# Kernel optimization log

Hardware: AMD Instinct MI355X
Metric: run time of the kernel (lower is better)

The kernel has to match this reference:

```python
import jax, jax.numpy as jnp
import numpy as np

E = 16          # num_local_experts
K = 4           # experts_per_token
H = 2048        # hidden_size
I = 2048        # intermediate_size
LIMIT = 7.0     # swiglu_limit
ALPHA = 1.702   # glu_alpha


def setup_inputs() -> dict:
    key = jax.random.key(0)
    ks = jax.random.split(key, 9)
    int8 = lambda k, shp: jax.random.randint(k, shp, -127, 128).astype(jnp.float32)
    return {
        "hidden_states": jax.random.normal(ks[0], (1024, H), dtype=jnp.float32),
        "router_logits": jax.random.normal(ks[1], (1024, E), dtype=jnp.float32),
        "gate_up_proj": int8(ks[2], (E, H, 2 * I)),                      # int8 values in f32
        "gate_up_proj_scale": jax.random.uniform(ks[3], (E, 2 * I), minval=0.5, maxval=1.5) * 0.002,
        "gate_up_proj_bias": jax.random.normal(ks[4], (E, 2 * I), dtype=jnp.float32) * 0.01,
        "gate_up_smooth_scale": jnp.ones((E, I), dtype=jnp.float32),
        "down_proj": int8(ks[5], (E, I, H)),
        "down_proj_scale": jax.random.uniform(ks[6], (E, H), minval=0.5, maxval=1.5) * 0.002,
        "down_proj_bias": jax.random.normal(ks[7], (E, H), dtype=jnp.float32) * 0.01,
    }


def _dyn_quant(x):
    # per-token symmetric int8 dynamic quant (npu_dynamic_quant)
    scale = jnp.maximum(jnp.max(jnp.abs(x), axis=-1, keepdims=True) / 127.0, 1e-8)
    q = jnp.clip(jnp.round(x / scale), -127.0, 127.0)
    return q, scale


def reference(hidden_states, router_logits, gate_up_proj, gate_up_proj_scale,
              gate_up_proj_bias, gate_up_smooth_scale, down_proj,
              down_proj_scale, down_proj_bias):
    T = hidden_states.shape[0]
    C = (2 * T * K) // E

    # --- gating (npu_moe_gating_top_k: softmax + top-k, then renormalize) ---
    probs = jax.nn.softmax(router_logits, axis=-1)
    topk_w, topk_i = jax.lax.top_k(probs, K)                 # [T,K]
    topk_w = topk_w / jnp.sum(topk_w, axis=-1, keepdims=True)

    # --- per-token dynamic quant ---
    x_q, x_scale = _dyn_quant(hidden_states)                 # [T,H], [T,1]

    # --- dispatch (npu_moe_init_routing_v2): token-major expansion, capacity buckets ---
    flat_e = topk_i.reshape(-1)                              # [T*K] expert id per row
    flat_w = topk_w.reshape(-1)                              # [T*K]
    src = jnp.arange(T * K) // K                             # [T*K] source token
    onehot = jax.nn.one_hot(flat_e, E, dtype=jnp.int32)      # [T*K,E]
    pos = jnp.sum(jnp.cumsum(onehot, axis=0) * onehot, axis=1) - 1  # position within expert
    valid = pos < C
    slot = flat_e * C + jnp.where(valid, pos, 0)             # unique for valid rows
    vf = valid.astype(x_q.dtype)[:, None]
    x_disp = jnp.zeros((E * C, H), x_q.dtype).at[slot].add(x_q[src] * vf)
    s_disp = jnp.zeros((E * C, 1), x_scale.dtype).at[slot].add(x_scale[src] * vf)
    x_disp = x_disp.reshape(E, C, H)
    s_disp = s_disp.reshape(E, C, 1)

    gu_i32 = jnp.einsum('ech,ehf->ecf', x_disp, gate_up_proj)          # [E,C,2I]
    y = gu_i32 * s_disp * gate_up_proj_scale[:, None, :] + gate_up_proj_bias[:, None, :]

    # --- gpt-oss swiglu (activate_left, clamp_limit, alpha=1.702, glu_bias=1.0) ---
    gate = jnp.minimum(y[..., :I], LIMIT)
    up = jnp.clip(y[..., I:], -LIMIT, LIMIT)
    act = gate * jax.nn.sigmoid(ALPHA * gate) * (up + 1.0)
    act = act * gate_up_smooth_scale[:, None, :]

    # --- requant + grouped GEMM 2 + dequant ---
    h_q, h_scale = _dyn_quant(act)                                     # [E,C,I], [E,C,1]
    z_i32 = jnp.einsum('eci,eih->ech', h_q, down_proj)                 # [E,C,H]
    z = z_i32 * h_scale * down_proj_scale[:, None, :] + down_proj_bias[:, None, :]

    # --- combine (npu_moe_finalize_routing): weighted scatter-add per source token ---
    gathered = z.reshape(E * C, H)[slot]                               # [T*K,H]
    out = jnp.zeros((T, H), z.dtype).at[src].add(flat_w[:, None] * vf * gathered)
    return out
```

## Files before the change

### kernel.cpp

```cpp
#include <hip/hip_runtime.h>
#include <stdint.h>
#include <stddef.h>

#define T_TOK 1024
#define NE    16
#define TOPK  4
#define HID   2048
#define INTER 2048
#define CAP   512
#define GLIMIT 7.0f
#define GALPHA 1.702f

#define BM  128
#define BK  32
#define LDP 40

typedef __attribute__((ext_vector_type(8))) _Float16 half8;
typedef __attribute__((ext_vector_type(4))) float     f32x4;

__global__ __launch_bounds__(256) void gating_kernel(
    const float* __restrict__ logits, int* __restrict__ topki, float* __restrict__ topkw)
{
    int t = blockIdx.x * 256 + threadIdx.x;
    if (t >= T_TOK) return;
    float l[NE];
#pragma unroll
    for (int e = 0; e < NE; e++) l[e] = logits[t * NE + e];
    unsigned used = 0;
    float val[TOPK]; int idx[TOPK];
#pragma unroll
    for (int k = 0; k < TOPK; k++) {
        float bv = -3.4e38f; int bi = 0;
#pragma unroll
        for (int e = 0; e < NE; e++) {
            bool ok = (((used >> e) & 1u) == 0u) && (l[e] > bv);
            bv = ok ? l[e] : bv;
            bi = ok ? e : bi;
        }
        used |= (1u << bi); idx[k] = bi; val[k] = bv;
    }
    float m = val[0];
    float s = 0.f, w[TOPK];
#pragma unroll
    for (int k = 0; k < TOPK; k++) { w[k] = expf(val[k] - m); s += w[k]; }
    float inv = 1.0f / s;
#pragma unroll
    for (int k = 0; k < TOPK; k++) { topki[t * TOPK + k] = idx[k]; topkw[t * TOPK + k] = w[k] * inv; }
}

__global__ __launch_bounds__(256) void quant_x_kernel(
    const float* __restrict__ x, _Float16* __restrict__ xq, float* __restrict__ xs)
{
    int t = blockIdx.x;
    const float* row = x + (size_t)t * HID;
    __shared__ float red[256];
    float amax = 0.f;
    for (int i = threadIdx.x; i < HID; i += 256) amax = fmaxf(amax, fabsf(row[i]));
    red[threadIdx.x] = amax; __syncthreads();
    for (int s = 128; s > 0; s >>= 1) {
        if (threadIdx.x < s) red[threadIdx.x] = fmaxf(red[threadIdx.x], red[threadIdx.x + s]);
        __syncthreads();
    }
    float scale = fmaxf(red[0] / 127.0f, 1e-8f);
    if (threadIdx.x == 0) xs[t] = scale;
    for (int i = threadIdx.x; i < HID; i += 256) {
        float q = rintf(row[i] / scale);
        q = fminf(fmaxf(q, -127.f), 127.f);
        xq[(size_t)t * HID + i] = (_Float16)q;
    }
}

__global__ __launch_bounds__(1024) void routing_kernel(
    const int* __restrict__ topki, const float* __restrict__ topkw,
    int* __restrict__ row_src, float* __restrict__ row_w, int* __restrict__ counts)
{
    int wv = threadIdx.x >> 6;
    int lane = threadIdx.x & 63;
    int base = 0;
    for (int r0 = 0; r0 < T_TOK * TOPK; r0 += 64) {
        int r = r0 + lane;
        int e = topki[r];
        unsigned long long mask = __ballot(e == wv);
        int pre = __popcll(mask & ((1ULL << lane) - 1ULL));
        if (e == wv) {
            int pos = base + pre;
            if (pos < CAP) {
                row_src[wv * CAP + pos] = r >> 2;
                row_w[wv * CAP + pos] = topkw[r];
            }
        }
        base += __popcll(mask);
    }
    if (lane == 0) counts[wv] = (base < CAP) ? base : CAP;
}

__global__ __launch_bounds__(256) void gemm1_kernel(
    const _Float16* __restrict__ xq, const float* __restrict__ xs,
    const int* __restrict__ row_src, const int* __restrict__ counts,
    const float* __restrict__ gup, const float* __restrict__ gus,
    const float* __restrict__ gub, const float* __restrict__ smo,
    float* __restrict__ act)
{
    int nt = blockIdx.x;
    int mt = blockIdx.y;
    int e  = blockIdx.z;
    int count = counts[e];
    int m0 = mt * BM;
    if (m0 >= count) return;

    __shared__ _Float16 sA[BM * LDP];
    __shared__ _Float16 sB[128 * LDP];

    int t = threadIdx.x;
    int lane = t & 63, w = t >> 6;
    int n16 = lane & 15, quad = lane >> 4;

    int aM = t >> 1, aHalf = t & 1;
    int agr = m0 + aM;
    const _Float16* aptr = nullptr;
    if (agr < count) aptr = xq + (size_t)row_src[e * CAP + agr] * HID;

    f32x4 acc[2][8];
#pragma unroll
    for (int i = 0; i < 2; i++)
#pragma unroll
        for (int j = 0; j < 8; j++) acc[i][j] = (f32x4)0.0f;

    const float* gbase = gup + (size_t)e * HID * (2 * INTER);

    for (int k0 = 0; k0 < HID; k0 += BK) {
        __syncthreads();
        {
            int4 v0, v1;
            v0.x = v0.y = v0.z = v0.w = 0; v1 = v0;
            if (aptr) {
                const int4* s4 = (const int4*)(aptr + k0 + aHalf * 16);
                v0 = s4[0]; v1 = s4[1];
            }
            int4* d4 = (int4*)&sA[aM * LDP + aHalf * 16];
            d4[0] = v0; d4[1] = v1;
        }
        {
            int n = t & 63;
            int kr = (t >> 6) * 8;
#pragma unroll
            for (int h = 0; h < 2; h++) {
                const float* src = gbase + (size_t)(k0 + kr) * (2 * INTER) + h * INTER + nt * 64 + n;
#pragma unroll
                for (int i = 0; i < 8; i++)
                    sB[(h * 64 + n) * LDP + kr + i] = (_Float16)src[(size_t)i * (2 * INTER)];
            }
        }
        __syncthreads();

        half8 af[2], bfr[8];
#pragma unroll
        for (int mf = 0; mf < 2; mf++)
            af[mf] = *(const half8*)&sA[(w * 32 + mf * 16 + n16) * LDP + quad * 8];
#pragma unroll
        for (int nf = 0; nf < 8; nf++)
            bfr[nf] = *(const half8*)&sB[(nf * 16 + n16) * LDP + quad * 8];
#pragma unroll
        for (int mf = 0; mf < 2; mf++)
#pragma unroll
            for (int nf = 0; nf < 8; nf++)
                acc[mf][nf] = __builtin_amdgcn_mfma_f32_16x16x32_f16(af[mf], bfr[nf], acc[mf][nf], 0, 0, 0);
    }

    const float* gsc = gus + (size_t)e * (2 * INTER);
    const float* gbi = gub + (size_t)e * (2 * INTER);
    const float* sms = smo + (size_t)e * INTER;
#pragma unroll
    for (int mf = 0; mf < 2; mf++) {
#pragma unroll
        for (int r = 0; r < 4; r++) {
            int gr = m0 + w * 32 + mf * 16 + quad * 4 + r;
            if (gr >= count) continue;
            float srow = xs[row_src[e * CAP + gr]];
            float* arow = act + (size_t)(e * CAP + gr) * INTER;
#pragma unroll
            for (int g = 0; g < 4; g++) {
                int col = nt * 64 + g * 16 + n16;
                float yg = acc[mf][g][r]     * srow * gsc[col]         + gbi[col];
                float yu = acc[mf][g + 4][r] * srow * gsc[INTER + col] + gbi[INTER + col];
                float gate = fminf(yg, GLIMIT);
                float up   = fminf(fmaxf(yu, -GLIMIT), GLIMIT);
                float sig  = 1.0f / (1.0f + expf(-GALPHA * gate));
                arow[col] = gate * sig * (up + 1.0f) * sms[col];
            }
        }
    }
}

__global__ __launch_bounds__(256) void requant_kernel(
    const float* __restrict__ act, const int* __restrict__ counts,
    _Float16* __restrict__ hq, float* __restrict__ hs)
{
    int b = blockIdx.x;
    int e = b >> 9, c = b & (CAP - 1);
    if (c >= counts[e]) return;
    const float* row = act + (size_t)b * INTER;
    __shared__ float red[256];
    float amax = 0.f;
    for (int i = threadIdx.x; i < INTER; i += 256) amax = fmaxf(amax, fabsf(row[i]));
    red[threadIdx.x] = amax; __syncthreads();
    for (int s = 128; s > 0; s >>= 1) {
        if (threadIdx.x < s) red[threadIdx.x] = fmaxf(red[threadIdx.x], red[threadIdx.x + s]);
        __syncthreads();
    }
    float scale = fmaxf(red[0] / 127.0f, 1e-8f);
    if (threadIdx.x == 0) hs[b] = scale;
    for (int i = threadIdx.x; i < INTER; i += 256) {
        float q = rintf(row[i] / scale);
        q = fminf(fmaxf(q, -127.f), 127.f);
        hq[(size_t)b * INTER + i] = (_Float16)q;
    }
}

__global__ __launch_bounds__(256) void gemm2_kernel(
    const _Float16* __restrict__ hq, const float* __restrict__ hs,
    const int* __restrict__ row_src, const float* __restrict__ row_w,
    const int* __restrict__ counts, const float* __restrict__ dwn,
    const float* __restrict__ dsc, const float* __restrict__ dbi,
    float* __restrict__ out)
{
    int nt = blockIdx.x;
    int mt = blockIdx.y;
    int e  = blockIdx.z;
    int count = counts[e];
    int m0 = mt * BM;
    if (m0 >= count) return;

    __shared__ _Float16 sA[BM * LDP];
    __shared__ _Float16 sB[128 * LDP];

    int t = threadIdx.x;
    int lane = t & 63, w = t >> 6;
    int n16 = lane & 15, quad = lane >> 4;

    int aM = t >> 1, aHalf = t & 1;
    int agr = m0 + aM;
    const _Float16* aptr = nullptr;
    if (agr < count) aptr = hq + (size_t)(e * CAP + agr) * INTER;

    f32x4 acc[2][8];
#pragma unroll
    for (int i = 0; i < 2; i++)
#pragma unroll
        for (int j = 0; j < 8; j++) acc[i][j] = (f32x4)0.0f;

    const float* bbase = dwn + (size_t)e * INTER * HID;

    for (int k0 = 0; k0 < INTER; k0 += BK) {
        __syncthreads();
        {
            int4 v0, v1;
            v0.x = v0.y = v0.z = v0.w = 0; v1 = v0;
            if (aptr) {
                const int4* s4 = (const int4*)(aptr + k0 + aHalf * 16);
                v0 = s4[0]; v1 = s4[1];
            }
            int4* d4 = (int4*)&sA[aM * LDP + aHalf * 16];
            d4[0] = v0; d4[1] = v1;
        }
        {
            int n = t & 127;
            int kr = (t >> 7) * 16;
            const float* src = bbase + (size_t)(k0 + kr) * HID + nt * 128 + n;
#pragma unroll
            for (int i = 0; i < 16; i++)
                sB[n * LDP + kr + i] = (_Float16)src[(size_t)i * HID];
        }
        __syncthreads();

        half8 af[2], bfr[8];
#pragma unroll
        for (int mf = 0; mf < 2; mf++)
            af[mf] = *(const half8*)&sA[(w * 32 + mf * 16 + n16) * LDP + quad * 8];
#pragma unroll
        for (int nf = 0; nf < 8; nf++)
            bfr[nf] = *(const half8*)&sB[(nf * 16 + n16) * LDP + quad * 8];
#pragma unroll
        for (int mf = 0; mf < 2; mf++)
#pragma unroll
            for (int nf = 0; nf < 8; nf++)
                acc[mf][nf] = __builtin_amdgcn_mfma_f32_16x16x32_f16(af[mf], bfr[nf], acc[mf][nf], 0, 0, 0);
    }

    const float* dscE = dsc + (size_t)e * HID;
    const float* dbiE = dbi + (size_t)e * HID;
#pragma unroll
    for (int mf = 0; mf < 2; mf++) {
#pragma unroll
        for (int r = 0; r < 4; r++) {
            int gr = m0 + w * 32 + mf * 16 + quad * 4 + r;
            if (gr >= count) continue;
            int ri = e * CAP + gr;
            float hsr = hs[ri];
            float wr  = row_w[ri];
            float* orow = out + (size_t)row_src[ri] * HID;
#pragma unroll
            for (int nf = 0; nf < 8; nf++) {
                int col = nt * 128 + nf * 16 + n16;
                float z = acc[mf][nf][r] * hsr * dscE[col] + dbiE[col];
                atomicAdd(&orow[col], wr * z);
            }
        }
    }
}

extern "C" void kernel_launch(void* const* d_in, const int* in_sizes, int n_in,
                              void* d_out, int out_size, void* d_ws, size_t ws_size,
                              hipStream_t stream)
{
    (void)in_sizes; (void)n_in; (void)out_size; (void)ws_size;
    const float* x   = (const float*)d_in[0];
    const float* rl  = (const float*)d_in[1];
    const float* gup = (const float*)d_in[2];
    const float* gus = (const float*)d_in[3];
    const float* gub = (const float*)d_in[4];
    const float* smo = (const float*)d_in[5];
    const float* dwn = (const float*)d_in[6];
    const float* dsc = (const float*)d_in[7];
    const float* dbi = (const float*)d_in[8];
    float* out = (float*)d_out;

    char* p = (char*)d_ws;
    auto carve = [&](size_t bytes) -> char* {
        char* r = p; p += (bytes + 255) & ~(size_t)255; return r;
    };
    _Float16* xq   = (_Float16*)carve((size_t)T_TOK * HID * 2);
    float* xs      = (float*)carve((size_t)T_TOK * 4);
    int* topki     = (int*)carve((size_t)T_TOK * TOPK * 4);
    float* topkw   = (float*)carve((size_t)T_TOK * TOPK * 4);
    int* counts    = (int*)carve((size_t)NE * 4);
    int* rsrc      = (int*)carve((size_t)NE * CAP * 4);
    float* rw      = (float*)carve((size_t)NE * CAP * 4);
    float* actb    = (float*)carve((size_t)NE * CAP * INTER * 4);
    _Float16* hq   = (_Float16*)carve((size_t)NE * CAP * INTER * 2);
    float* hsb     = (float*)carve((size_t)NE * CAP * 4);

    hipMemsetAsync(d_out, 0, (size_t)T_TOK * HID * 4, stream);
    gating_kernel<<<dim3((T_TOK + 255) / 256), 256, 0, stream>>>(rl, topki, topkw);
    quant_x_kernel<<<dim3(T_TOK), 256, 0, stream>>>(x, xq, xs);
    routing_kernel<<<dim3(1), 1024, 0, stream>>>(topki, topkw, rsrc, rw, counts);
    gemm1_kernel<<<dim3(INTER / 64, CAP / BM, NE), 256, 0, stream>>>(
        xq, xs, rsrc, counts, gup, gus, gub, smo, actb);
    requant_kernel<<<dim3(NE * CAP), 256, 0, stream>>>(actb, counts, hq, hsb);
    gemm2_kernel<<<dim3(HID / 128, CAP / BM, NE), 256, 0, stream>>>(
        hq, hsb, rsrc, rw, counts, dwn, dsc, dbi, out);
}
```

Baseline: 1.078 ms.

## Retile MoE GEMMs to 256-row M tiles with vectorized weight loads and warp skipping

Both grouped GEMMs now use 512-thread blocks with a 256-row M tile, BK of 64 and a 64-column N tile. The f32 weight tiles are loaded as coalesced float4 rows and packed as half2 pairs into LDS, replacing the strided per-element scalar loads. Because the M tile covers the whole expected token count, the weight matrices are streamed fewer times per expert. Warps whose rows lie beyond the expert's count skip their MFMA work. Costs are more LDS per block, fewer MFMAs per wave per K-step, and possible LDS bank conflicts from the transposed half2 stores.

```diff
diff --git a/kernel.cpp b/kernel.cpp
--- a/kernel.cpp
+++ b/kernel.cpp
@@ -11,11 +11,13 @@
 #define GLIMIT 7.0f
 #define GALPHA 1.702f
 
-#define BM  128
-#define BK  32
-#define LDP 40
+#define BM  256
+#define BK  64
+#define PA  88
+#define PB  88
 
 typedef __attribute__((ext_vector_type(8))) _Float16 half8;
+typedef __attribute__((ext_vector_type(2))) _Float16 half2v;
 typedef __attribute__((ext_vector_type(4))) float     f32x4;
 
 __global__ __launch_bounds__(256) void gating_kernel(
@@ -94,7 +96,7 @@
     if (lane == 0) counts[wv] = (base < CAP) ? base : CAP;
 }
 
-__global__ __launch_bounds__(256) void gemm1_kernel(
+__global__ __launch_bounds__(512) void gemm1_kernel(
     const _Float16* __restrict__ xq, const float* __restrict__ xs,
     const int* __restrict__ row_src, const int* __restrict__ counts,
     const float* __restrict__ gup, const float* __restrict__ gus,
@@ -108,65 +110,82 @@
     int m0 = mt * BM;
     if (m0 >= count) return;
 
-    __shared__ _Float16 sA[BM * LDP];
-    __shared__ _Float16 sB[128 * LDP];
+    __shared__ _Float16 sA[BM * PA];
+    __shared__ _Float16 sB[64 * PB];
 
     int t = threadIdx.x;
     int lane = t & 63, w = t >> 6;
     int n16 = lane & 15, quad = lane >> 4;
 
-    int aM = t >> 1, aHalf = t & 1;
-    int agr = m0 + aM;
+    int arow = t >> 1, ahalf = t & 1;
     const _Float16* aptr = nullptr;
-    if (agr < count) aptr = xq + (size_t)row_src[e * CAP + agr] * HID;
-
-    f32x4 acc[2][8];
+    {
+        int agr = m0 + arow;
+        if (agr < count) aptr = xq + (size_t)row_src[e * CAP + agr] * HID;
+    }
+    _Float16* sAw = &sA[arow * PA + ahalf * 32];
+
+    int colq = t & 15;
+    int kp   = t >> 4;
+    int c64  = colq * 4;
+    const float* bptr = gup + (size_t)e * HID * (2 * INTER)
+                      + (size_t)(c64 >> 5) * INTER + nt * 32 + (c64 & 31);
+    _Float16* sBw = &sB[c64 * PB + kp * 2];
+
+    f32x4 acc[2][4];
 #pragma unroll
     for (int i = 0; i < 2; i++)
 #pragma unroll
-        for (int j = 0; j < 8; j++) acc[i][j] = (f32x4)0.0f;
-
-    const float* gbase = gup + (size_t)e * HID * (2 * INTER);
+        for (int j = 0; j < 4; j++) acc[i][j] = (f32x4)0.0f;
+
+    bool wactive = (m0 + w * 32) < count;
 
     for (int k0 = 0; k0 < HID; k0 += BK) {
         __syncthreads();
         {
-            int4 v0, v1;
-            v0.x = v0.y = v0.z = v0.w = 0; v1 = v0;
+            int4 v0 = {0,0,0,0}, v1 = v0, v2 = v0, v3 = v0;
             if (aptr) {
-                const int4* s4 = (const int4*)(aptr + k0 + aHalf * 16);
-                v0 = s4[0]; v1 = s4[1];
-            }
-            int4* d4 = (int4*)&sA[aM * LDP + aHalf * 16];
-            d4[0] = v0; d4[1] = v1;
+                const int4* s4 = (const int4*)(aptr + k0 + ahalf * 32);
+                v0 = s4[0]; v1 = s4[1]; v2 = s4[2]; v3 = s4[3];
+            }
+            int4* d = (int4*)sAw;
+            d[0] = v0; d[1] = v1; d[2] = v2; d[3] = v3;
         }
         {
-            int n = t & 63;
-            int kr = (t >> 6) * 8;
-#pragma unroll
-            for (int h = 0; h < 2; h++) {
-                const float* src = gbase + (size_t)(k0 + kr) * (2 * INTER) + h * INTER + nt * 64 + n;
-#pragma unroll
-                for (int i = 0; i < 8; i++)
-                    sB[(h * 64 + n) * LDP + kr + i] = (_Float16)src[(size_t)i * (2 * INTER)];
-            }
-        }
-        __syncthreads();
-
-        half8 af[2], bfr[8];
-#pragma unroll
-        for (int mf = 0; mf < 2; mf++)
-            af[mf] = *(const half8*)&sA[(w * 32 + mf * 16 + n16) * LDP + quad * 8];
-#pragma unroll
-        for (int nf = 0; nf < 8; nf++)
-            bfr[nf] = *(const half8*)&sB[(nf * 16 + n16) * LDP + quad * 8];
-#pragma unroll
-        for (int mf = 0; mf < 2; mf++)
-#pragma unroll
-            for (int nf = 0; nf < 8; nf++)
-                acc[mf][nf] = __builtin_amdgcn_mfma_f32_16x16x32_f16(af[mf], bfr[nf], acc[mf][nf], 0, 0, 0);
-    }
-
+            const float* s = bptr + (size_t)(k0 + kp * 2) * (2 * INTER);
+            float4 r0 = *(const float4*)(s);
+            float4 r1 = *(const float4*)(s + 2 * INTER);
+            half2v w0 = { (_Float16)r0.x, (_Float16)r1.x };
+            half2v w1 = { (_Float16)r0.y, (_Float16)r1.y };
+            half2v w2 = { (_Float16)r0.z, (_Float16)r1.z };
+            half2v w3 = { (_Float16)r0.w, (_Float16)r1.w };
+            *(half2v*)(sBw + 0 * PB) = w0;
+            *(half2v*)(sBw + 1 * PB) = w1;
+            *(half2v*)(sBw + 2 * PB) = w2;
+            *(half2v*)(sBw + 3 * PB) = w3;
+        }
+        __syncthreads();
+
+        if (wactive) {
+#pragma unroll
+            for (int ks = 0; ks < 2; ks++) {
+                half8 af[2], bfr[4];
+#pragma unroll
+                for (int mf = 0; mf < 2; mf++)
+                    af[mf] = *(const half8*)&sA[(w * 32 + mf * 16 + n16) * PA + ks * 32 + quad * 8];
+#pragma unroll
+                for (int nf = 0; nf < 4; nf++)
+                    bfr[nf] = *(const half8*)&sB[(nf * 16 + n16) * PB + ks * 32 + quad * 8];
+#pragma unroll
+                for (int mf = 0; mf < 2; mf++)
+#pragma unroll
+                    for (int nf = 0; nf < 4; nf++)
+                        acc[mf][nf] = __builtin_amdgcn_mfma_f32_16x16x32_f16(af[mf], bfr[nf], acc[mf][nf], 0, 0, 0);
+            }
+        }
+    }
+
+    if (!wactive) return;
     const float* gsc = gus + (size_t)e * (2 * INTER);
     const float* gbi = gub + (size_t)e * (2 * INTER);
     const float* sms = smo + (size_t)e * INTER;
@@ -177,16 +196,16 @@
             int gr = m0 + w * 32 + mf * 16 + quad * 4 + r;
             if (gr >= count) continue;
             float srow = xs[row_src[e * CAP + gr]];
-            float* arow = act + (size_t)(e * CAP + gr) * INTER;
-#pragma unroll
-            for (int g = 0; g < 4; g++) {
-                int col = nt * 64 + g * 16 + n16;
+            float* arow_p = act + (size_t)(e * CAP + gr) * INTER;
+#pragma unroll
+            for (int g = 0; g < 2; g++) {
+                int col = nt * 32 + g * 16 + n16;
                 float yg = acc[mf][g][r]     * srow * gsc[col]         + gbi[col];
-                float yu = acc[mf][g + 4][r] * srow * gsc[INTER + col] + gbi[INTER + col];
+                float yu = acc[mf][g + 2][r] * srow * gsc[INTER + col] + gbi[INTER + col];
                 float gate = fminf(yg, GLIMIT);
                 float up   = fminf(fmaxf(yu, -GLIMIT), GLIMIT);
                 float sig  = 1.0f / (1.0f + expf(-GALPHA * gate));
-                arow[col] = gate * sig * (up + 1.0f) * sms[col];
+                arow_p[col] = gate * sig * (up + 1.0f) * sms[col];
             }
         }
     }
@@ -217,7 +236,7 @@
     }
 }
 
-__global__ __launch_bounds__(256) void gemm2_kernel(
+__global__ __launch_bounds__(512) void gemm2_kernel(
     const _Float16* __restrict__ hq, const float* __restrict__ hs,
     const int* __restrict__ row_src, const float* __restrict__ row_w,
     const int* __restrict__ counts, const float* __restrict__ dwn,
@@ -231,62 +250,81 @@
     int m0 = mt * BM;
     if (m0 >= count) return;
 
-    __shared__ _Float16 sA[BM * LDP];
-    __shared__ _Float16 sB[128 * LDP];
+    __shared__ _Float16 sA[BM * PA];
+    __shared__ _Float16 sB[64 * PB];
 
     int t = threadIdx.x;
     int lane = t & 63, w = t >> 6;
     int n16 = lane & 15, quad = lane >> 4;
 
-    int aM = t >> 1, aHalf = t & 1;
-    int agr = m0 + aM;
+    int arow = t >> 1, ahalf = t & 1;
     const _Float16* aptr = nullptr;
-    if (agr < count) aptr = hq + (size_t)(e * CAP + agr) * INTER;
-
-    f32x4 acc[2][8];
+    {
+        int agr = m0 + arow;
+        if (agr < count) aptr = hq + (size_t)(e * CAP + agr) * INTER;
+    }
+    _Float16* sAw = &sA[arow * PA + ahalf * 32];
+
+    int colq = t & 15;
+    int kp   = t >> 4;
+    int c64  = colq * 4;
+    const float* bptr = dwn + (size_t)e * INTER * HID + nt * 64 + c64;
+    _Float16* sBw = &sB[c64 * PB + kp * 2];
+
+    f32x4 acc[2][4];
 #pragma unroll
     for (int i = 0; i < 2; i++)
 #pragma unroll
-        for (int j = 0; j < 8; j++) acc[i][j] = (f32x4)0.0f;
-
-    const float* bbase = dwn + (size_t)e * INTER * HID;
+        for (int j = 0; j < 4; j++) acc[i][j] = (f32x4)0.0f;
+
+    bool wactive = (m0 + w * 32) < count;
 
     for (int k0 = 0; k0 < INTER; k0 += BK) {
         __syncthreads();
         {
-            int4 v0, v1;
-            v0.x = v0.y = v0.z = v0.w = 0; v1 = v0;
+            int4 v0 = {0,0,0,0}, v1 = v0, v2 = v0, v3 = v0;
             if (aptr) {
-                const int4* s4 = (const int4*)(aptr + k0 + aHalf * 16);
-                v0 = s4[0]; v1 = s4[1];
-            }
-            int4* d4 = (int4*)&sA[aM * LDP + aHalf * 16];
-            d4[0] = v0; d4[1] = v1;
+                const int4* s4 = (const int4*)(aptr + k0 + ahalf * 32);
+                v0 = s4[0]; v1 = s4[1]; v2 = s4[2]; v3 = s4[3];
+            }
+            int4* d = (int4*)sAw;
+            d[0] = v0; d[1] = v1; d[2] = v2; d[3] = v3;
         }
         {
-            int n = t & 127;
-            int kr = (t >> 7) * 16;
-            const float* src = bbase + (size_t)(k0 + kr) * HID + nt * 128 + n;
-#pragma unroll
-            for (int i = 0; i < 16; i++)
-                sB[n * LDP + kr + i] = (_Float16)src[(size_t)i * HID];
-        }
-        __syncthreads();
-
-        half8 af[2], bfr[8];
-#pragma unroll
-        for (int mf = 0; mf < 2; mf++)
-            af[mf] = *(const half8*)&sA[(w * 32 + mf * 16 + n16) * LDP + quad * 8];
-#pragma unroll
-        for (int nf = 0; nf < 8; nf++)
-            bfr[nf] = *(const half8*)&sB[(nf * 16 + n16) * LDP + quad * 8];
-#pragma unroll
-        for (int mf = 0; mf < 2; mf++)
-#pragma unroll
-            for (int nf = 0; nf < 8; nf++)
-                acc[mf][nf] = __builtin_amdgcn_mfma_f32_16x16x32_f16(af[mf], bfr[nf], acc[mf][nf], 0, 0, 0);
-    }
-
+            const float* s = bptr + (size_t)(k0 + kp * 2) * HID;
+            float4 r0 = *(const float4*)(s);
+            float4 r1 = *(const float4*)(s + HID);
+            half2v w0 = { (_Float16)r0.x, (_Float16)r1.x };
+            half2v w1 = { (_Float16)r0.y, (_Float16)r1.y };
+            half2v w2 = { (_Float16)r0.z, (_Float16)r1.z };
+            half2v w3 = { (_Float16)r0.w, (_Float16)r1.w };
+            *(half2v*)(sBw + 0 * PB) = w0;
+            *(half2v*)(sBw + 1 * PB) = w1;
+            *(half2v*)(sBw + 2 * PB) = w2;
+            *(half2v*)(sBw + 3 * PB) = w3;
+        }
+        __syncthreads();
+
+        if (wactive) {
+#pragma unroll
+            for (int ks = 0; ks < 2; ks++) {
+                half8 af[2], bfr[4];
+#pragma unroll
+                for (int mf = 0; mf < 2; mf++)
+                    af[mf] = *(const half8*)&sA[(w * 32 + mf * 16 + n16) * PA + ks * 32 + quad * 8];
+#pragma unroll
+                for (int nf = 0; nf < 4; nf++)
+                    bfr[nf] = *(const half8*)&sB[(nf * 16 + n16) * PB + ks * 32 + quad * 8];
+#pragma unroll
+                for (int mf = 0; mf < 2; mf++)
+#pragma unroll
+                    for (int nf = 0; nf < 4; nf++)
+                        acc[mf][nf] = __builtin_amdgcn_mfma_f32_16x16x32_f16(af[mf], bfr[nf], acc[mf][nf], 0, 0, 0);
+            }
+        }
+    }
+
+    if (!wactive) return;
     const float* dscE = dsc + (size_t)e * HID;
     const float* dbiE = dbi + (size_t)e * HID;
 #pragma unroll
@@ -300,8 +338,8 @@
             float wr  = row_w[ri];
             float* orow = out + (size_t)row_src[ri] * HID;
 #pragma unroll
-            for (int nf = 0; nf < 8; nf++) {
-                int col = nt * 128 + nf * 16 + n16;
+            for (int nf = 0; nf < 4; nf++) {
+                int col = nt * 64 + nf * 16 + n16;
                 float z = acc[mf][nf][r] * hsr * dscE[col] + dbiE[col];
                 atomicAdd(&orow[col], wr * z);
             }
@@ -344,9 +382,9 @@
     gating_kernel<<<dim3((T_TOK + 255) / 256), 256, 0, stream>>>(rl, topki, topkw);
     quant_x_kernel<<<dim3(T_TOK), 256, 0, stream>>>(x, xq, xs);
     routing_kernel<<<dim3(1), 1024, 0, stream>>>(topki, topkw, rsrc, rw, counts);
-    gemm1_kernel<<<dim3(INTER / 64, CAP / BM, NE), 256, 0, stream>>>(
+    gemm1_kernel<<<dim3(INTER / 32, 2, NE), 512, 0, stream>>>(
         xq, xs, rsrc, counts, gup, gus, gub, smo, actb);
     requant_kernel<<<dim3(NE * CAP), 256, 0, stream>>>(actb, counts, hq, hsb);
-    gemm2_kernel<<<dim3(HID / 128, CAP / BM, NE), 256, 0, stream>>>(
+    gemm2_kernel<<<dim3(HID / 64, 2, NE), 512, 0, stream>>>(
         hq, hsb, rsrc, rw, counts, dwn, dsc, dbi, out);
 }
```

Result: slower. 1.115 ms (+3.4%).
